# Performance work log

Measured on AMD Instinct MI355X. Metric: run time of the kernel, lower is better.

The kernel has to match this reference:

```python
import jax, jax.numpy as jnp
import numpy as np

B, LA, LS, C, H = 4, 1536, 512, 256, 4
DK = C // H
NEG = -jnp.inf


def _pad(lengths, maxlen):
    # True where padded (idx >= length)
    return jnp.arange(maxlen)[None, :] >= lengths[:, None]


def build_mask(l_v, l_s, ilens, ylens):
    """Additive float mask [B, l_v+l_s, l_v+l_s] with 0 / -inf, matching
    generate_multi_modal_mask_new."""
    b = ilens.shape[0]
    i = jnp.arange(l_s)
    causal = jnp.where(i[:, None] >= i[None, :], 0.0, NEG)            # [l_s, l_s]
    tgt_pad = _pad(ylens, l_s)                                        # [b, l_s]
    mask_s_s = jnp.where(tgt_pad[:, None, :], NEG, causal[None])      # [b, l_s, l_s]
    src_row = jnp.where(_pad(ilens, l_v), NEG, 0.0)                   # [b, l_v]
    mask_v_v = jnp.broadcast_to(src_row[:, None, :], (b, l_v, l_v))
    mask_s_v = jnp.broadcast_to(src_row[:, None, :], (b, l_s, l_v))
    mask_v_s = jnp.full((b, l_v, l_s), NEG, dtype=jnp.float32)
    top = jnp.concatenate([mask_v_v, mask_v_s], axis=2)
    bot = jnp.concatenate([mask_s_v, mask_s_s], axis=2)
    return jnp.concatenate([top, bot], axis=1)


def setup_inputs() -> dict:
    key = jax.random.key(0)
    ks = jax.random.split(key, 12)
    scale = 1.0 / np.sqrt(C)
    return {
        "audio_encoder_out": jax.random.normal(ks[0], (B, LA, C), jnp.float32),
        "text_encoder_out": jax.random.normal(ks[1], (B, LS, C), jnp.float32),
        "speech_length": jax.random.randint(ks[2], (B,), 1, LA),
        "text_length": jax.random.randint(ks[3], (B,), 1, LS),
        "Wq": jax.random.normal(ks[4], (C, C), jnp.float32) * scale,
        "bq": jax.random.normal(ks[5], (C,), jnp.float32) * scale,
        "Wk": jax.random.normal(ks[6], (C, C), jnp.float32) * scale,
        "bk": jax.random.normal(ks[7], (C,), jnp.float32) * scale,
        "Wv": jax.random.normal(ks[8], (C, C), jnp.float32) * scale,
        "bv": jax.random.normal(ks[9], (C,), jnp.float32) * scale,
        "Wo": jax.random.normal(ks[10], (C, C), jnp.float32) * scale,
        "bo": jax.random.normal(ks[11], (C,), jnp.float32) * scale,
    }


def reference(audio_encoder_out, text_encoder_out, speech_length, text_length,
              Wq, bq, Wk, bk, Wv, bv, Wo, bo):
    b, l_a, c = audio_encoder_out.shape
    l_s = text_encoder_out.shape[1]
    x = jnp.concatenate([audio_encoder_out, text_encoder_out], axis=1)  # [B, L, C]
    L = l_a + l_s

    def heads(W, bias):
        return (x @ W.T + bias).reshape(b, L, H, DK).transpose(0, 2, 1, 3)  # [B,H,L,DK]

    q, k, v = heads(Wq, bq), heads(Wk, bk), heads(Wv, bv)
    scores = jnp.einsum("bhqd,bhkd->bhqk", q, k) / np.float32(np.sqrt(DK))

    amask = build_mask(l_a, l_s, speech_length, text_length)  # additive [B,L,L]
    # Faithful to torch: mask.eq(0) positions (additive-0) are filled with -inf,
    # then zeroed in attn (the module's inverted masking behavior).
    eq0 = (amask == 0.0)[:, None, :, :]                       # [B,1,L,L]
    scores = jnp.where(eq0, NEG, scores)
    attn = jax.nn.softmax(scores, axis=-1)
    attn = jnp.where(eq0, 0.0, attn)                          # (dropout = identity, eval)
    out = jnp.einsum("bhqk,bhkd->bhqd", attn, v)
    out = out.transpose(0, 2, 1, 3).reshape(b, L, H * DK)
    return out @ Wo.T + bo
```

## Files before the change

### kernel.cpp

```cpp
#include <hip/hip_runtime.h>
#include <hip/hip_bf16.h>
#include <math.h>

#define LA 1536
#define LS 512
#define LT 2048
#define CC 256
#define NH 4
#define DKH 64
#define NB 4
#define NT (LT / 64)
#define NTA (LA / 64)

typedef _Float16 f16;
typedef __attribute__((ext_vector_type(8))) _Float16 f16x8;
typedef __attribute__((ext_vector_type(4))) _Float16 f16x4;
typedef __attribute__((ext_vector_type(4))) float f32x4;

__device__ inline f16x8 cvt8(const float4 a, const float4 b) {
    f16x8 h;
    h[0] = (_Float16)a.x; h[1] = (_Float16)a.y; h[2] = (_Float16)a.z; h[3] = (_Float16)a.w;
    h[4] = (_Float16)b.x; h[5] = (_Float16)b.y; h[6] = (_Float16)b.z; h[7] = (_Float16)b.w;
    return h;
}

__global__ __launch_bounds__(256) void qkv_mfma(
    const float* __restrict__ audio, const float* __restrict__ text,
    const float* __restrict__ Wq, const float* __restrict__ bq,
    const float* __restrict__ Wk, const float* __restrict__ bk,
    const float* __restrict__ Wv, const float* __restrict__ bv,
    f16* __restrict__ Qh, f16* __restrict__ Kh, f16* __restrict__ Vth)
{
    __shared__ f16 smem[128 * 64 + 64 * 64];
    f16* As = smem;
    f16* Bs = smem + 128 * 64;

    const int tid = threadIdx.x;
    const int w = tid >> 6, l = tid & 63;
    const int g = l >> 4, r = l & 15;

    const int m0 = blockIdx.x * 128;
    const int n0 = blockIdx.y * 64;
    const int mat = n0 >> 8;
    const int ch0 = n0 & 255;

    const float* W    = (mat == 0) ? Wq : (mat == 1) ? Wk : Wv;
    const float* bias = (mat == 0) ? bq : (mat == 1) ? bk : bv;

    const int b  = m0 >> 11;
    const int l0 = m0 & 2047;

    f32x4 acc[2][4] = {};

    for (int k0 = 0; k0 < CC; k0 += 64) {
        #pragma unroll
        for (int m = 0; m < 4; ++m) {
            const int idx = m * 256 + tid;
            const int row = idx >> 3, c = idx & 7;
            const int lrow = l0 + row;
            const float* src = (lrow < LA)
                ? (audio + ((size_t)b * LA + lrow) * CC + k0 + c * 8)
                : (text  + ((size_t)b * LS + (lrow - LA)) * CC + k0 + c * 8);
            const float4 x0 = *(const float4*)src;
            const float4 x1 = *(const float4*)(src + 4);
            *(f16x8*)(As + row * 64 + ((c ^ (row & 7)) << 3)) = cvt8(x0, x1);
        }
        #pragma unroll
        for (int m = 0; m < 2; ++m) {
            const int idx = m * 256 + tid;
            const int row = idx >> 3, c = idx & 7;
            const float* src = W + (size_t)(ch0 + row) * CC + k0 + c * 8;
            const float4 x0 = *(const float4*)src;
            const float4 x1 = *(const float4*)(src + 4);
            *(f16x8*)(Bs + row * 64 + ((c ^ (row & 7)) << 3)) = cvt8(x0, x1);
        }
        __syncthreads();
        #pragma unroll
        for (int kc = 0; kc < 2; ++kc) {
            f16x8 af[2];
            #pragma unroll
            for (int i = 0; i < 2; ++i) {
                const int row = w * 32 + i * 16 + r;
                const int c = kc * 4 + g;
                af[i] = *(const f16x8*)(As + row * 64 + ((c ^ (row & 7)) << 3));
            }
            f16x8 bf[4];
            #pragma unroll
            for (int j = 0; j < 4; ++j) {
                const int row = j * 16 + r;
                const int c = kc * 4 + g;
                bf[j] = *(const f16x8*)(Bs + row * 64 + ((c ^ (row & 7)) << 3));
            }
            #pragma unroll
            for (int i = 0; i < 2; ++i)
                #pragma unroll
                for (int j = 0; j < 4; ++j)
                    acc[i][j] = __builtin_amdgcn_mfma_f32_16x16x32_f16(af[i], bf[j], acc[i][j], 0, 0, 0);
        }
        __syncthreads();
    }

    float bcol[4];
    #pragma unroll
    for (int j = 0; j < 4; ++j) bcol[j] = bias[ch0 + j * 16 + r];

    if (mat <= 1) {
        f16* Out = (mat == 0) ? Qh : Kh;
        #pragma unroll
        for (int i = 0; i < 2; ++i)
            #pragma unroll
            for (int e = 0; e < 4; ++e) {
                const int m = m0 + w * 32 + i * 16 + g * 4 + e;
                #pragma unroll
                for (int j = 0; j < 4; ++j)
                    Out[(size_t)m * CC + ch0 + j * 16 + r] = (_Float16)(acc[i][j][e] + bcol[j]);
            }
    } else {
        f16* Ts = smem;
        #pragma unroll
        for (int i = 0; i < 2; ++i)
            #pragma unroll
            for (int e = 0; e < 4; ++e) {
                const int ml = w * 32 + i * 16 + g * 4 + e;
                #pragma unroll
                for (int j = 0; j < 4; ++j)
                    Ts[(j * 16 + r) * 136 + ml] = (_Float16)(acc[i][j][e] + bcol[j]);
            }
        __syncthreads();
        const int b2 = m0 >> 11, l0m = m0 & 2047;
        #pragma unroll
        for (int u = 0; u < 4; ++u) {
            const int idx = u * 256 + tid;
            const int nl = idx >> 4, mc = idx & 15;
            const f16x8 vv = *(const f16x8*)(Ts + nl * 136 + mc * 8);
            const int nglob = ch0 + nl;
            const int hh = nglob >> 6, dd = nglob & 63;
            *(f16x8*)(Vth + ((size_t)((b2 * NH + hh) * DKH + dd)) * LT + l0m + mc * 8) = vv;
        }
    }
}

__global__ __launch_bounds__(512) void attn_f16(
    const f16* __restrict__ Q, const f16* __restrict__ K,
    const f16* __restrict__ Vt,
    const int* __restrict__ slen, const int* __restrict__ tlen,
    f16* __restrict__ AO)
{
    __shared__ f16 Ks[2][4096];
    __shared__ f16 Vts[2][4096];
    __shared__ f16 Ps[8][16 * 72];
    __shared__ float Oc[4][1024];
    __shared__ float ML[2][64][2];

    const int tid = threadIdx.x;
    const int w = tid >> 6, l = tid & 63;
    const int gid = w >> 2, wg = w & 3;
    const int g = l >> 4, r = l & 15;
    const int tg = tid & 255;

    const int q0 = blockIdx.x * 64;
    const int h  = blockIdx.y;
    const int b  = blockIdx.z;

    const int ilen = slen[b];
    const int kcap = LA + tlen[b];
    const int nskip = ilen >> 6;
    int ntskip = 0;
    if (q0 >= LA) {
        const int skipmax = min(q0 - 63, kcap - 64);
        const int d = skipmax - LA;
        ntskip = (d < 0) ? 0 : ((d >> 6) + 1);
    }
    const int nAudio = NTA - nskip;
    const int nProc  = nAudio + (NT - NTA) - ntskip;
    const int nIter  = (nProc + 1) >> 1;

    const int qrow = q0 + 16 * wg + r;

    f16x8 qf[2];
    #pragma unroll
    for (int ch = 0; ch < 2; ++ch) {
        f16x8 q8 = *(const f16x8*)(Q + ((size_t)(b * LT) + qrow) * CC + h * DKH + ch * 32 + g * 8);
        #pragma unroll
        for (int e = 0; e < 8; ++e) q8[e] = q8[e] * (_Float16)0.125f;
        qf[ch] = q8;
    }

    const int srow0 = tg >> 3, scc = tg & 7;
    const int srow1 = srow0 + 32;
    const int sdst0 = srow0 * 64 + ((scc ^ (srow0 & 7)) << 3);
    const int sdst1 = srow1 * 64 + ((scc ^ (srow1 & 7)) << 3);

    #define TILE_OF(p) ((p) < nAudio ? (nskip + (p)) : (NTA + ntskip + ((p) - nAudio)))

    {
        const int k0 = TILE_OF(gid) * 64;
        *(f16x8*)(Ks[gid] + sdst0)  = *(const f16x8*)(K  + ((size_t)(b * LT) + k0 + srow0) * CC + h * DKH + scc * 8);
        *(f16x8*)(Vts[gid] + sdst0) = *(const f16x8*)(Vt + ((size_t)((b * NH + h) * DKH) + srow0) * LT + k0 + scc * 8);
        *(f16x8*)(Ks[gid] + sdst1)  = *(const f16x8*)(K  + ((size_t)(b * LT) + k0 + srow1) * CC + h * DKH + scc * 8);
        *(f16x8*)(Vts[gid] + sdst1) = *(const f16x8*)(Vt + ((size_t)((b * NH + h) * DKH) + srow1) * LT + k0 + scc * 8);
    }

    float m_run = -1e30f, l_run = 0.0f;
    f32x4 o[4] = {};

    for (int i = 0; i < nIter; ++i) {
        __syncthreads();
        const int pcur = 2 * i + gid;
        const bool curV = pcur < nProc;
        const bool nxtV = (pcur + 2) < nProc;

        f16x8 kr0, vr0, kr1, vr1;
        if (nxtV) {
            const int kn = TILE_OF(pcur + 2) * 64;
            kr0 = *(const f16x8*)(K  + ((size_t)(b * LT) + kn + srow0) * CC + h * DKH + scc * 8);
            vr0 = *(const f16x8*)(Vt + ((size_t)((b * NH + h) * DKH) + srow0) * LT + kn + scc * 8);
            kr1 = *(const f16x8*)(K  + ((size_t)(b * LT) + kn + srow1) * CC + h * DKH + scc * 8);
            vr1 = *(const f16x8*)(Vt + ((size_t)((b * NH + h) * DKH) + srow1) * LT + kn + scc * 8);
        }

        if (curV) {
            const int kt = TILE_OF(pcur);
            const int k0 = kt * 64;

            f32x4 sacc[4] = {};
            #pragma unroll
            for (int s = 0; s < 4; ++s) {
                const int row = 16 * s + r;
                #pragma unroll
                for (int ch = 0; ch < 2; ++ch) {
                    const f16x8 a = *(const f16x8*)(Ks[gid] + row * 64 + ((((ch * 4 + g) ^ (row & 7)) & 7) << 3));
                    sacc[s] = __builtin_amdgcn_mfma_f32_16x16x32_f16(a, qf[ch], sacc[s], 0, 0, 0);
                }
            }

            const int mode = (kt < NTA) ? ((k0 >= ilen) ? 0 : 1)
                                        : ((q0 < LA) ? 0 : 2);
            float sv[16];
            if (mode == 0) {
                #pragma unroll
                for (int s = 0; s < 4; ++s)
                    #pragma unroll
                    for (int e = 0; e < 4; ++e) sv[s * 4 + e] = sacc[s][e];
            } else if (mode == 1) {
                #pragma unroll
                for (int s = 0; s < 4; ++s)
                    #pragma unroll
                    for (int e = 0; e < 4; ++e) {
                        const int kk = k0 + 16 * s + 4 * g + e;
                        sv[s * 4 + e] = (kk >= ilen) ? sacc[s][e] : -INFINITY;
                    }
            } else {
                #pragma unroll
                for (int s = 0; s < 4; ++s)
                    #pragma unroll
                    for (int e = 0; e < 4; ++e) {
                        const int kk = k0 + 16 * s + 4 * g + e;
                        sv[s * 4 + e] = (kk > qrow || kk >= kcap) ? sacc[s][e] : -INFINITY;
                    }
            }

            float mloc = -1e30f;
            #pragma unroll
            for (int u = 0; u < 16; ++u) mloc = fmaxf(mloc, sv[u]);
            mloc = fmaxf(mloc, __shfl_xor(mloc, 16));
            mloc = fmaxf(mloc, __shfl_xor(mloc, 32));
            const float m_new = fmaxf(m_run, mloc);

            float ssum = 0.0f;
            f16x4 ph[4];
            #pragma unroll
            for (int s = 0; s < 4; ++s)
                #pragma unroll
                for (int e = 0; e < 4; ++e) {
                    const float p = __expf(sv[s * 4 + e] - m_new);
                    ph[s][e] = (_Float16)p;
                    ssum += p;
                }
            ssum += __shfl_xor(ssum, 16);
            ssum += __shfl_xor(ssum, 32);
            const float sc = __expf(m_run - m_new);
            l_run = l_run * sc + ssum;
            m_run = m_new;

            #pragma unroll
            for (int s = 0; s < 4; ++s)
                *(f16x4*)(&Ps[w][0] + r * 72 + 16 * s + 4 * g) = ph[s];

            #pragma unroll
            for (int e = 0; e < 4; ++e) {
                const float scr = __shfl(sc, 4 * g + e);
                #pragma unroll
                for (int dsb = 0; dsb < 4; ++dsb) o[dsb][e] *= scr;
            }

            #pragma unroll
            for (int ch = 0; ch < 2; ++ch) {
                const f16x8 a = *(const f16x8*)(&Ps[w][0] + r * 72 + ch * 32 + g * 8);
                #pragma unroll
                for (int dsb = 0; dsb < 4; ++dsb) {
                    const int vrow = 16 * dsb + r;
                    const f16x8 bf = *(const f16x8*)(Vts[gid] + vrow * 64 + ((((ch * 4 + g) ^ (vrow & 7)) & 7) << 3));
                    o[dsb] = __builtin_amdgcn_mfma_f32_16x16x32_f16(a, bf, o[dsb], 0, 0, 0);
                }
            }
        }

        __syncthreads();
        if (nxtV) {
            *(f16x8*)(Ks[gid] + sdst0)  = kr0;
            *(f16x8*)(Vts[gid] + sdst0) = vr0;
            *(f16x8*)(Ks[gid] + sdst1)  = kr1;
            *(f16x8*)(Vts[gid] + sdst1) = vr1;
        }
    }

    if (g == 0) {
        ML[gid][16 * wg + r][0] = m_run;
        ML[gid][16 * wg + r][1] = l_run;
    }
    if (gid == 1) {
        #pragma unroll
        for (int dsb = 0; dsb < 4; ++dsb)
            *(f32x4*)&Oc[wg][dsb * 256 + (g * 16 + r) * 4] = o[dsb];
    }
    __syncthreads();

    if (gid == 0) {
        #pragma unroll
        for (int e = 0; e < 4; ++e) {
            const int qloc = 16 * wg + 4 * g + e;
            const float m0v = ML[0][qloc][0], l0v = ML[0][qloc][1];
            const float m1v = ML[1][qloc][0], l1v = ML[1][qloc][1];
            const float mt = fmaxf(m0v, m1v);
            const float c0 = __expf(m0v - mt);
            const float c1 = __expf(m1v - mt);
            const float inv = 1.0f / (l0v * c0 + l1v * c1);
            const int qq = q0 + qloc;
            #pragma unroll
            for (int dsb = 0; dsb < 4; ++dsb) {
                const float of = (o[dsb][e] * c0 + Oc[wg][dsb * 256 + (g * 16 + r) * 4 + e] * c1) * inv;
                AO[((size_t)(b * LT) + qq) * CC + h * DKH + 16 * dsb + r] = (_Float16)of;
            }
        }
    }
    #undef TILE_OF
}

__global__ __launch_bounds__(256) void out_mfma(
    const f16* __restrict__ X, const float* __restrict__ Wo,
    const float* __restrict__ bo, float* __restrict__ Out)
{
    __shared__ f16 As[128 * 64];
    __shared__ f16 Bs[64 * 64];

    const int tid = threadIdx.x;
    const int w = tid >> 6, l = tid & 63;
    const int g = l >> 4, r = l & 15;

    const int m0 = blockIdx.x * 128;
    const int n0 = blockIdx.y * 64;

    f32x4 acc[2][4] = {};

    for (int k0 = 0; k0 < CC; k0 += 64) {
        #pragma unroll
        for (int m = 0; m < 4; ++m) {
            const int idx = m * 256 + tid;
            const int row = idx >> 3, c = idx & 7;
            *(f16x8*)(As + row * 64 + ((c ^ (row & 7)) << 3)) =
                *(const f16x8*)(X + (size_t)(m0 + row) * CC + k0 + c * 8);
        }
        #pragma unroll
        for (int m = 0; m < 2; ++m) {
            const int idx = m * 256 + tid;
            const int row = idx >> 3, c = idx & 7;
            const float* src = Wo + (size_t)(n0 + row) * CC + k0 + c * 8;
            const float4 x0 = *(const float4*)src;
            const float4 x1 = *(const float4*)(src + 4);
            *(f16x8*)(Bs + row * 64 + ((c ^ (row & 7)) << 3)) = cvt8(x0, x1);
        }
        __syncthreads();
        #pragma unroll
        for (int kc = 0; kc < 2; ++kc) {
            f16x8 af[2];
            #pragma unroll
            for (int i = 0; i < 2; ++i) {
                const int row = w * 32 + i * 16 + r;
                const int c = kc * 4 + g;
                af[i] = *(const f16x8*)(As + row * 64 + ((c ^ (row & 7)) << 3));
            }
            f16x8 bf[4];
            #pragma unroll
            for (int j = 0; j < 4; ++j) {
                const int row = j * 16 + r;
                const int c = kc * 4 + g;
                bf[j] = *(const f16x8*)(Bs + row * 64 + ((c ^ (row & 7)) << 3));
            }
            #pragma unroll
            for (int i = 0; i < 2; ++i)
                #pragma unroll
                for (int j = 0; j < 4; ++j)
                    acc[i][j] = __builtin_amdgcn_mfma_f32_16x16x32_f16(af[i], bf[j], acc[i][j], 0, 0, 0);
        }
        __syncthreads();
    }

    float bcol[4];
    #pragma unroll
    for (int j = 0; j < 4; ++j) bcol[j] = bo[n0 + j * 16 + r];

    #pragma unroll
    for (int i = 0; i < 2; ++i)
        #pragma unroll
        for (int e = 0; e < 4; ++e) {
            const int m = m0 + w * 32 + i * 16 + g * 4 + e;
            #pragma unroll
            for (int j = 0; j < 4; ++j)
                Out[(size_t)m * CC + n0 + j * 16 + r] = acc[i][j][e] + bcol[j];
        }
}

extern "C" void kernel_launch(void* const* d_in, const int* in_sizes, int n_in,
                              void* d_out, int out_size, void* d_ws, size_t ws_size,
                              hipStream_t stream)
{
    const float* audio = (const float*)d_in[0];
    const float* text  = (const float*)d_in[1];
    const int*   slen  = (const int*)d_in[2];
    const int*   tlen  = (const int*)d_in[3];
    const float* Wq = (const float*)d_in[4];
    const float* bq = (const float*)d_in[5];
    const float* Wk = (const float*)d_in[6];
    const float* bk = (const float*)d_in[7];
    const float* Wv = (const float*)d_in[8];
    const float* bv = (const float*)d_in[9];
    const float* Wo = (const float*)d_in[10];
    const float* bo = (const float*)d_in[11];
    float* out = (float*)d_out;

    const size_t SZ = (size_t)NB * LT * CC;
    f16* Qh  = (f16*)d_ws;
    f16* Kh  = Qh + SZ;
    f16* Vth = Kh + SZ;
    f16* AOh = Vth + SZ;

    qkv_mfma<<<dim3(64, 12), 256, 0, stream>>>(audio, text, Wq, bq, Wk, bk, Wv, bv,
                                               Qh, Kh, Vth);
    attn_f16<<<dim3(LT / 64, NH, NB), 512, 0, stream>>>(Qh, Kh, Vth, slen, tlen, AOh);
    out_mfma<<<dim3(64, 4), 256, 0, stream>>>(AOh, Wo, bo, out);
}
```

Before: 49.30 us.

## Give each attention wave two query subtiles, fold scale into Q, use exp2

The attention kernel drops from 512 to 256 threads per block, and each wave now handles 32 query rows instead of 16. This reuses every K and V fragment read from shared memory across two MFMA chains, halving the LDS read traffic per unit of work. The softmax scale times log2(e) is folded into the Q projection epilogue, so the kernel can use exp2f and skip the per-load Q scaling. Rescaling of the running output is skipped when the running max is unchanged across the wave, and the merge buffers now alias the P buffer to cut shared memory. In exchange, register pressure per thread rises and there are fewer waves per block to hide latency.

After: 59.55 us. +20.8%, slower.

```diff
diff --git a/kernel.cpp b/kernel.cpp
--- a/kernel.cpp
+++ b/kernel.cpp
@@ -11,6 +11,9 @@
 #define NB 4
 #define NT (LT / 64)
 #define NTA (LA / 64)
+#define SZ ((size_t)NB * LT * CC)
+
+#define QSCALE 0.1803368801111244f
 
 typedef _Float16 f16;
 typedef __attribute__((ext_vector_type(8))) _Float16 f16x8;
@@ -106,6 +109,7 @@
 
     if (mat <= 1) {
         f16* Out = (mat == 0) ? Qh : Kh;
+        const float osc = (mat == 0) ? QSCALE : 1.0f;
         #pragma unroll
         for (int i = 0; i < 2; ++i)
             #pragma unroll
@@ -113,7 +117,8 @@
                 const int m = m0 + w * 32 + i * 16 + g * 4 + e;
                 #pragma unroll
                 for (int j = 0; j < 4; ++j)
-                    Out[(size_t)m * CC + ch0 + j * 16 + r] = (_Float16)(acc[i][j][e] + bcol[j]);
+                    Out[(size_t)m * CC + ch0 + j * 16 + r] =
+                        (_Float16)((acc[i][j][e] + bcol[j]) * osc);
             }
     } else {
         f16* Ts = smem;
@@ -140,7 +145,7 @@
     }
 }
 
-__global__ __launch_bounds__(512) void attn_f16(
+__global__ __launch_bounds__(256) void attn_f16(
     const f16* __restrict__ Q, const f16* __restrict__ K,
     const f16* __restrict__ Vt,
     const int* __restrict__ slen, const int* __restrict__ tlen,
@@ -148,15 +153,12 @@
 {
     __shared__ f16 Ks[2][4096];
     __shared__ f16 Vts[2][4096];
-    __shared__ f16 Ps[8][16 * 72];
-    __shared__ float Oc[4][1024];
-    __shared__ float ML[2][64][2];
+    __shared__ __align__(16) f16 Ps[4][2304];
 
     const int tid = threadIdx.x;
     const int w = tid >> 6, l = tid & 63;
-    const int gid = w >> 2, wg = w & 3;
+    const int gid = w >> 1, wg = w & 1;
     const int g = l >> 4, r = l & 15;
-    const int tg = tid & 255;
 
     const int q0 = blockIdx.x * 64;
     const int h  = blockIdx.y;
@@ -175,34 +177,37 @@
     const int nProc  = nAudio + (NT - NTA) - ntskip;
     const int nIter  = (nProc + 1) >> 1;
 
-    const int qrow = q0 + 16 * wg + r;
-
-    f16x8 qf[2];
+    const int qbase = q0 + 32 * wg;
+
+    f16x8 qf[2][2];
     #pragma unroll
-    for (int ch = 0; ch < 2; ++ch) {
-        f16x8 q8 = *(const f16x8*)(Q + ((size_t)(b * LT) + qrow) * CC + h * DKH + ch * 32 + g * 8);
-        #pragma unroll
-        for (int e = 0; e < 8; ++e) q8[e] = q8[e] * (_Float16)0.125f;
-        qf[ch] = q8;
-    }
-
-    const int srow0 = tg >> 3, scc = tg & 7;
-    const int srow1 = srow0 + 32;
-    const int sdst0 = srow0 * 64 + ((scc ^ (srow0 & 7)) << 3);
-    const int sdst1 = srow1 * 64 + ((scc ^ (srow1 & 7)) << 3);
+    for (int j = 0; j < 2; ++j)
+        #pragma unroll
+        for (int ch = 0; ch < 2; ++ch)
+            qf[j][ch] = *(const f16x8*)(Q + ((size_t)(b * LT) + qbase + 16 * j + r) * CC
+                                        + h * DKH + ch * 32 + g * 8);
+
+    const int tg = tid & 127;
+    const int rowb = tg >> 3, scc = tg & 7;
+    const int c2 = ((scc ^ (rowb & 7)) << 3);
+    const int sbase = rowb * 64 + c2;
 
     #define TILE_OF(p) ((p) < nAudio ? (nskip + (p)) : (NTA + ntskip + ((p) - nAudio)))
 
     {
         const int k0 = TILE_OF(gid) * 64;
-        *(f16x8*)(Ks[gid] + sdst0)  = *(const f16x8*)(K  + ((size_t)(b * LT) + k0 + srow0) * CC + h * DKH + scc * 8);
-        *(f16x8*)(Vts[gid] + sdst0) = *(const f16x8*)(Vt + ((size_t)((b * NH + h) * DKH) + srow0) * LT + k0 + scc * 8);
-        *(f16x8*)(Ks[gid] + sdst1)  = *(const f16x8*)(K  + ((size_t)(b * LT) + k0 + srow1) * CC + h * DKH + scc * 8);
-        *(f16x8*)(Vts[gid] + sdst1) = *(const f16x8*)(Vt + ((size_t)((b * NH + h) * DKH) + srow1) * LT + k0 + scc * 8);
-    }
-
-    float m_run = -1e30f, l_run = 0.0f;
-    f32x4 o[4] = {};
+        #pragma unroll
+        for (int u = 0; u < 4; ++u) {
+            const int row = u * 16 + rowb;
+            *(f16x8*)(Ks[gid] + u * 1024 + sbase) =
+                *(const f16x8*)(K + ((size_t)(b * LT) + k0 + row) * CC + h * DKH + scc * 8);
+            *(f16x8*)(Vts[gid] + u * 1024 + sbase) =
+                *(const f16x8*)(Vt + ((size_t)((b * NH + h) * DKH) + row) * LT + k0 + scc * 8);
+        }
+    }
+
+    float m_run[2] = {-1e30f, -1e30f}, l_run[2] = {0.0f, 0.0f};
+    f32x4 o[4][2] = {};
 
     for (int i = 0; i < nIter; ++i) {
         __syncthreads();
@@ -210,137 +215,166 @@
         const bool curV = pcur < nProc;
         const bool nxtV = (pcur + 2) < nProc;
 
-        f16x8 kr0, vr0, kr1, vr1;
+        f16x8 kr[4], vr[4];
         if (nxtV) {
             const int kn = TILE_OF(pcur + 2) * 64;
-            kr0 = *(const f16x8*)(K  + ((size_t)(b * LT) + kn + srow0) * CC + h * DKH + scc * 8);
-            vr0 = *(const f16x8*)(Vt + ((size_t)((b * NH + h) * DKH) + srow0) * LT + kn + scc * 8);
-            kr1 = *(const f16x8*)(K  + ((size_t)(b * LT) + kn + srow1) * CC + h * DKH + scc * 8);
-            vr1 = *(const f16x8*)(Vt + ((size_t)((b * NH + h) * DKH) + srow1) * LT + kn + scc * 8);
+            #pragma unroll
+            for (int u = 0; u < 4; ++u) {
+                const int row = u * 16 + rowb;
+                kr[u] = *(const f16x8*)(K + ((size_t)(b * LT) + kn + row) * CC + h * DKH + scc * 8);
+                vr[u] = *(const f16x8*)(Vt + ((size_t)((b * NH + h) * DKH) + row) * LT + kn + scc * 8);
+            }
         }
 
         if (curV) {
             const int kt = TILE_OF(pcur);
             const int k0 = kt * 64;
 
-            f32x4 sacc[4] = {};
+            f32x4 sacc[4][2] = {};
             #pragma unroll
             for (int s = 0; s < 4; ++s) {
-                const int row = 16 * s + r;
+                const int arow = 16 * s + r;
                 #pragma unroll
                 for (int ch = 0; ch < 2; ++ch) {
-                    const f16x8 a = *(const f16x8*)(Ks[gid] + row * 64 + ((((ch * 4 + g) ^ (row & 7)) & 7) << 3));
-                    sacc[s] = __builtin_amdgcn_mfma_f32_16x16x32_f16(a, qf[ch], sacc[s], 0, 0, 0);
+                    const f16x8 a = *(const f16x8*)(Ks[gid] + arow * 64 + ((((ch * 4 + g) ^ (arow & 7)) & 7) << 3));
+                    #pragma unroll
+                    for (int j = 0; j < 2; ++j)
+                        sacc[s][j] = __builtin_amdgcn_mfma_f32_16x16x32_f16(a, qf[j][ch], sacc[s][j], 0, 0, 0);
                 }
             }
 
             const int mode = (kt < NTA) ? ((k0 >= ilen) ? 0 : 1)
                                         : ((q0 < LA) ? 0 : 2);
-            float sv[16];
-            if (mode == 0) {
+
+            #pragma unroll
+            for (int j = 0; j < 2; ++j) {
+                const int qrow = qbase + 16 * j + r;
+                float sv[16];
+                if (mode == 0) {
+                    #pragma unroll
+                    for (int s = 0; s < 4; ++s)
+                        #pragma unroll
+                        for (int e = 0; e < 4; ++e) sv[s * 4 + e] = sacc[s][j][e];
+                } else if (mode == 1) {
+                    #pragma unroll
+                    for (int s = 0; s < 4; ++s)
+                        #pragma unroll
+                        for (int e = 0; e < 4; ++e) {
+                            const int kk = k0 + 16 * s + 4 * g + e;
+                            sv[s * 4 + e] = (kk >= ilen) ? sacc[s][j][e] : -INFINITY;
+                        }
+                } else {
+                    #pragma unroll
+                    for (int s = 0; s < 4; ++s)
+                        #pragma unroll
+                        for (int e = 0; e < 4; ++e) {
+                            const int kk = k0 + 16 * s + 4 * g + e;
+                            sv[s * 4 + e] = (kk > qrow || kk >= kcap) ? sacc[s][j][e] : -INFINITY;
+                        }
+                }
+
+                float mloc = -1e30f;
+                #pragma unroll
+                for (int u = 0; u < 16; ++u) mloc = fmaxf(mloc, sv[u]);
+                mloc = fmaxf(mloc, __shfl_xor(mloc, 16));
+                mloc = fmaxf(mloc, __shfl_xor(mloc, 32));
+                const float m_new = fmaxf(m_run[j], mloc);
+
+                float ssum = 0.0f;
+                f16x4 ph[4];
                 #pragma unroll
                 for (int s = 0; s < 4; ++s)
                     #pragma unroll
-                    for (int e = 0; e < 4; ++e) sv[s * 4 + e] = sacc[s][e];
-            } else if (mode == 1) {
+                    for (int e = 0; e < 4; ++e) {
+                        const float p = exp2f(sv[s * 4 + e] - m_new);
+                        ph[s][e] = (_Float16)p;
+                        ssum += p;
+                    }
+                ssum += __shfl_xor(ssum, 16);
+                ssum += __shfl_xor(ssum, 32);
+
+                if (__all(m_new == m_run[j])) {
+                    l_run[j] += ssum;
+                } else {
+                    const float sc = exp2f(m_run[j] - m_new);
+                    l_run[j] = l_run[j] * sc + ssum;
+                    m_run[j] = m_new;
+                    #pragma unroll
+                    for (int e = 0; e < 4; ++e) {
+                        const float scr = __shfl(sc, 4 * g + e);
+                        #pragma unroll
+                        for (int dsb = 0; dsb < 4; ++dsb) o[dsb][j][e] *= scr;
+                    }
+                }
+
                 #pragma unroll
                 for (int s = 0; s < 4; ++s)
-                    #pragma unroll
-                    for (int e = 0; e < 4; ++e) {
-                        const int kk = k0 + 16 * s + 4 * g + e;
-                        sv[s * 4 + e] = (kk >= ilen) ? sacc[s][e] : -INFINITY;
-                    }
-            } else {
-                #pragma unroll
-                for (int s = 0; s < 4; ++s)
-                    #pragma unroll
-                    for (int e = 0; e < 4; ++e) {
-                        const int kk = k0 + 16 * s + 4 * g + e;
-                        sv[s * 4 + e] = (kk > qrow || kk >= kcap) ? sacc[s][e] : -INFINITY;
-                    }
-            }
-
-            float mloc = -1e30f;
-            #pragma unroll
-            for (int u = 0; u < 16; ++u) mloc = fmaxf(mloc, sv[u]);
-            mloc = fmaxf(mloc, __shfl_xor(mloc, 16));
-            mloc = fmaxf(mloc, __shfl_xor(mloc, 32));
-            const float m_new = fmaxf(m_run, mloc);
-
-            float ssum = 0.0f;
-            f16x4 ph[4];
-            #pragma unroll
-            for (int s = 0; s < 4; ++s)
-                #pragma unroll
-                for (int e = 0; e < 4; ++e) {
-                    const float p = __expf(sv[s * 4 + e] - m_new);
-                    ph[s][e] = (_Float16)p;
-                    ssum += p;
-                }
-            ssum += __shfl_xor(ssum, 16);
-            ssum += __shfl_xor(ssum, 32);
-            const float sc = __expf(m_run - m_new);
-            l_run = l_run * sc + ssum;
-            m_run = m_new;
-
-            #pragma unroll
-            for (int s = 0; s < 4; ++s)
-                *(f16x4*)(&Ps[w][0] + r * 72 + 16 * s + 4 * g) = ph[s];
-
-            #pragma unroll
-            for (int e = 0; e < 4; ++e) {
-                const float scr = __shfl(sc, 4 * g + e);
-                #pragma unroll
-                for (int dsb = 0; dsb < 4; ++dsb) o[dsb][e] *= scr;
+                    *(f16x4*)(&Ps[w][0] + (16 * j + r) * 72 + 16 * s + 4 * g) = ph[s];
             }
 
             #pragma unroll
             for (int ch = 0; ch < 2; ++ch) {
-                const f16x8 a = *(const f16x8*)(&Ps[w][0] + r * 72 + ch * 32 + g * 8);
+                f16x8 a[2];
+                #pragma unroll
+                for (int j = 0; j < 2; ++j)
+                    a[j] = *(const f16x8*)(&Ps[w][0] + (16 * j + r) * 72 + ch * 32 + g * 8);
                 #pragma unroll
                 for (int dsb = 0; dsb < 4; ++dsb) {
                     const int vrow = 16 * dsb + r;
                     const f16x8 bf = *(const f16x8*)(Vts[gid] + vrow * 64 + ((((ch * 4 + g) ^ (vrow & 7)) & 7) << 3));
-                    o[dsb] = __builtin_amdgcn_mfma_f32_16x16x32_f16(a, bf, o[dsb], 0, 0, 0);
+                    #pragma unroll
+                    for (int j = 0; j < 2; ++j)
+                        o[dsb][j] = __builtin_amdgcn_mfma_f32_16x16x32_f16(a[j], bf, o[dsb][j], 0, 0, 0);
                 }
             }
         }
 
         __syncthreads();
         if (nxtV) {
-            *(f16x8*)(Ks[gid] + sdst0)  = kr0;
-            *(f16x8*)(Vts[gid] + sdst0) = vr0;
-            *(f16x8*)(Ks[gid] + sdst1)  = kr1;
-            *(f16x8*)(Vts[gid] + sdst1) = vr1;
-        }
-    }
-
-    if (g == 0) {
-        ML[gid][16 * wg + r][0] = m_run;
-        ML[gid][16 * wg + r][1] = l_run;
-    }
+            #pragma unroll
+            for (int u = 0; u < 4; ++u) {
+                *(f16x8*)(Ks[gid] + u * 1024 + sbase) = kr[u];
+                *(f16x8*)(Vts[gid] + u * 1024 + sbase) = vr[u];
+            }
+        }
+    }
+
+    float* OcF = (float*)&Ps[0][0];
+    float* ML1 = OcF + 4096;
     if (gid == 1) {
         #pragma unroll
-        for (int dsb = 0; dsb < 4; ++dsb)
-            *(f32x4*)&Oc[wg][dsb * 256 + (g * 16 + r) * 4] = o[dsb];
+        for (int j = 0; j < 2; ++j) {
+            #pragma unroll
+            for (int dsb = 0; dsb < 4; ++dsb)
+                *(f32x4*)(OcF + (((wg * 2 + j) * 4 + dsb) << 8) + (l << 2)) = o[dsb][j];
+            if (g == 0) {
+                ML1[(32 * wg + 16 * j + r) * 2 + 0] = m_run[j];
+                ML1[(32 * wg + 16 * j + r) * 2 + 1] = l_run[j];
+            }
+        }
     }
     __syncthreads();
 
     if (gid == 0) {
         #pragma unroll
-        for (int e = 0; e < 4; ++e) {
-            const int qloc = 16 * wg + 4 * g + e;
-            const float m0v = ML[0][qloc][0], l0v = ML[0][qloc][1];
-            const float m1v = ML[1][qloc][0], l1v = ML[1][qloc][1];
-            const float mt = fmaxf(m0v, m1v);
-            const float c0 = __expf(m0v - mt);
-            const float c1 = __expf(m1v - mt);
-            const float inv = 1.0f / (l0v * c0 + l1v * c1);
-            const int qq = q0 + qloc;
-            #pragma unroll
-            for (int dsb = 0; dsb < 4; ++dsb) {
-                const float of = (o[dsb][e] * c0 + Oc[wg][dsb * 256 + (g * 16 + r) * 4 + e] * c1) * inv;
-                AO[((size_t)(b * LT) + qq) * CC + h * DKH + 16 * dsb + r] = (_Float16)of;
+        for (int j = 0; j < 2; ++j) {
+            #pragma unroll
+            for (int e = 0; e < 4; ++e) {
+                const int qloc = 32 * wg + 16 * j + 4 * g + e;
+                const float m0v = __shfl(m_run[j], 4 * g + e);
+                const float l0v = __shfl(l_run[j], 4 * g + e);
+                const float m1v = ML1[qloc * 2 + 0];
+                const float l1v = ML1[qloc * 2 + 1];
+                const float mt = fmaxf(m0v, m1v);
+                const float c0 = exp2f(m0v - mt);
+                const float c1 = exp2f(m1v - mt);
+                const float inv = 1.0f / (l0v * c0 + l1v * c1);
+                #pragma unroll
+                for (int dsb = 0; dsb < 4; ++dsb) {
+                    const float v = (o[dsb][j][e] * c0
+                                   + OcF[(((wg * 2 + j) * 4 + dsb) << 8) + (l << 2) + e] * c1) * inv;
+                    AO[((size_t)(b * LT) + q0 + qloc) * CC + h * DKH + 16 * dsb + r] = (_Float16)v;
+                }
             }
         }
     }
@@ -439,7 +473,6 @@
     const float* bo = (const float*)d_in[11];
     float* out = (float*)d_out;
 
-    const size_t SZ = (size_t)NB * LT * CC;
     f16* Qh  = (f16*)d_ws;
     f16* Kh  = Qh + SZ;
     f16* Vth = Kh + SZ;
@@ -447,6 +480,6 @@
 
     qkv_mfma<<<dim3(64, 12), 256, 0, stream>>>(audio, text, Wq, bq, Wk, bk, Wv, bv,
                                                Qh, Kh, Vth);
-    attn_f16<<<dim3(LT / 64, NH, NB), 512, 0, stream>>>(Qh, Kh, Vth, slen, tlen, AOh);
+    attn_f16<<<dim3(LT / 64, NH, NB), 256, 0, stream>>>(Qh, Kh, Vth, slen, tlen, AOh);
     out_mfma<<<dim3(64, 4), 256, 0, stream>>>(AOh, Wo, bo, out);
 }
```

## Keep P in registers via K row permutation, double-buffer K/V, fold scale into Q

Applied to the files above, without the earlier changes.

Q is pre-scaled by log2(e)/sqrt(dk) in the projection kernel so attention can use exp2 with no per-load scaling. K rows are stored in LDS in a permuted order so the score MFMA output lines up with the PV MFMA A-operand layout. That lets P stay in registers and removes the Ps shared-memory round trip. K/V tiles get a real double buffer with one barrier per iteration instead of two. The output rescale is skipped when no row max changes, and LDS is reused for the final merge. The trade-offs are more shared memory and a more complex index permutation.

New measurement: 51.13 us. +3.7%, slower.

```diff
diff --git a/kernel.cpp b/kernel.cpp
--- a/kernel.cpp
+++ b/kernel.cpp
@@ -11,6 +11,9 @@
 #define NB 4
 #define NT (LT / 64)
 #define NTA (LA / 64)
+#define SZ ((size_t)NB * LT * CC)
+
+#define QSCALE 0.1803368801111244f
 
 typedef _Float16 f16;
 typedef __attribute__((ext_vector_type(8))) _Float16 f16x8;
@@ -23,6 +26,8 @@
     h[4] = (_Float16)b.x; h[5] = (_Float16)b.y; h[6] = (_Float16)b.z; h[7] = (_Float16)b.w;
     return h;
 }
+
+#define PROW(j) (((j) & 32) | ((((j) >> 2) & 1) << 4) | ((((j) >> 3) & 3) << 2) | ((j) & 3))
 
 __global__ __launch_bounds__(256) void qkv_mfma(
     const float* __restrict__ audio, const float* __restrict__ text,
@@ -106,6 +111,7 @@
 
     if (mat <= 1) {
         f16* Out = (mat == 0) ? Qh : Kh;
+        const float osc = (mat == 0) ? QSCALE : 1.0f;
         #pragma unroll
         for (int i = 0; i < 2; ++i)
             #pragma unroll
@@ -113,7 +119,8 @@
                 const int m = m0 + w * 32 + i * 16 + g * 4 + e;
                 #pragma unroll
                 for (int j = 0; j < 4; ++j)
-                    Out[(size_t)m * CC + ch0 + j * 16 + r] = (_Float16)(acc[i][j][e] + bcol[j]);
+                    Out[(size_t)m * CC + ch0 + j * 16 + r] =
+                        (_Float16)((acc[i][j][e] + bcol[j]) * osc);
             }
     } else {
         f16* Ts = smem;
@@ -146,11 +153,8 @@
     const int* __restrict__ slen, const int* __restrict__ tlen,
     f16* __restrict__ AO)
 {
-    __shared__ f16 Ks[2][4096];
-    __shared__ f16 Vts[2][4096];
-    __shared__ f16 Ps[8][16 * 72];
-    __shared__ float Oc[4][1024];
-    __shared__ float ML[2][64][2];
+    __shared__ __align__(16) f16 KsA[2][2 * 4096];
+    __shared__ __align__(16) f16 VtsA[2][2 * 4096];
 
     const int tid = threadIdx.x;
     const int w = tid >> 6, l = tid & 63;
@@ -179,63 +183,70 @@
 
     f16x8 qf[2];
     #pragma unroll
-    for (int ch = 0; ch < 2; ++ch) {
-        f16x8 q8 = *(const f16x8*)(Q + ((size_t)(b * LT) + qrow) * CC + h * DKH + ch * 32 + g * 8);
-        #pragma unroll
-        for (int e = 0; e < 8; ++e) q8[e] = q8[e] * (_Float16)0.125f;
-        qf[ch] = q8;
-    }
+    for (int ch = 0; ch < 2; ++ch)
+        qf[ch] = *(const f16x8*)(Q + ((size_t)(b * LT) + qrow) * CC + h * DKH + ch * 32 + g * 8);
 
     const int srow0 = tg >> 3, scc = tg & 7;
     const int srow1 = srow0 + 32;
-    const int sdst0 = srow0 * 64 + ((scc ^ (srow0 & 7)) << 3);
-    const int sdst1 = srow1 * 64 + ((scc ^ (srow1 & 7)) << 3);
+    const int kp0 = PROW(srow0), kp1 = PROW(srow1);
+    const int kdst0 = kp0 * 64 + ((scc ^ (kp0 & 7)) << 3);
+    const int kdst1 = kp1 * 64 + ((scc ^ (kp1 & 7)) << 3);
+    const int vdst0 = srow0 * 64 + ((scc ^ (srow0 & 7)) << 3);
+    const int vdst1 = srow1 * 64 + ((scc ^ (srow1 & 7)) << 3);
 
     #define TILE_OF(p) ((p) < nAudio ? (nskip + (p)) : (NTA + ntskip + ((p) - nAudio)))
 
     {
         const int k0 = TILE_OF(gid) * 64;
-        *(f16x8*)(Ks[gid] + sdst0)  = *(const f16x8*)(K  + ((size_t)(b * LT) + k0 + srow0) * CC + h * DKH + scc * 8);
-        *(f16x8*)(Vts[gid] + sdst0) = *(const f16x8*)(Vt + ((size_t)((b * NH + h) * DKH) + srow0) * LT + k0 + scc * 8);
-        *(f16x8*)(Ks[gid] + sdst1)  = *(const f16x8*)(K  + ((size_t)(b * LT) + k0 + srow1) * CC + h * DKH + scc * 8);
-        *(f16x8*)(Vts[gid] + sdst1) = *(const f16x8*)(Vt + ((size_t)((b * NH + h) * DKH) + srow1) * LT + k0 + scc * 8);
-    }
+        *(f16x8*)(KsA[gid] + kdst0) =
+            *(const f16x8*)(K + ((size_t)(b * LT) + k0 + srow0) * CC + h * DKH + scc * 8);
+        *(f16x8*)(KsA[gid] + kdst1) =
+            *(const f16x8*)(K + ((size_t)(b * LT) + k0 + srow1) * CC + h * DKH + scc * 8);
+        *(f16x8*)(VtsA[gid] + vdst0) =
+            *(const f16x8*)(Vt + ((size_t)((b * NH + h) * DKH) + srow0) * LT + k0 + scc * 8);
+        *(f16x8*)(VtsA[gid] + vdst1) =
+            *(const f16x8*)(Vt + ((size_t)((b * NH + h) * DKH) + srow1) * LT + k0 + scc * 8);
+    }
+    __syncthreads();
 
     float m_run = -1e30f, l_run = 0.0f;
     f32x4 o[4] = {};
 
+    int cur = 0;
     for (int i = 0; i < nIter; ++i) {
-        __syncthreads();
         const int pcur = 2 * i + gid;
         const bool curV = pcur < nProc;
         const bool nxtV = (pcur + 2) < nProc;
 
-        f16x8 kr0, vr0, kr1, vr1;
+        f16x8 kr0, kr1, vr0, vr1;
         if (nxtV) {
             const int kn = TILE_OF(pcur + 2) * 64;
-            kr0 = *(const f16x8*)(K  + ((size_t)(b * LT) + kn + srow0) * CC + h * DKH + scc * 8);
+            kr0 = *(const f16x8*)(K + ((size_t)(b * LT) + kn + srow0) * CC + h * DKH + scc * 8);
+            kr1 = *(const f16x8*)(K + ((size_t)(b * LT) + kn + srow1) * CC + h * DKH + scc * 8);
             vr0 = *(const f16x8*)(Vt + ((size_t)((b * NH + h) * DKH) + srow0) * LT + kn + scc * 8);
-            kr1 = *(const f16x8*)(K  + ((size_t)(b * LT) + kn + srow1) * CC + h * DKH + scc * 8);
             vr1 = *(const f16x8*)(Vt + ((size_t)((b * NH + h) * DKH) + srow1) * LT + kn + scc * 8);
         }
 
         if (curV) {
             const int kt = TILE_OF(pcur);
             const int k0 = kt * 64;
+            const f16* Kb = KsA[gid] + cur * 4096;
+            const f16* Vb = VtsA[gid] + cur * 4096;
 
             f32x4 sacc[4] = {};
             #pragma unroll
             for (int s = 0; s < 4; ++s) {
-                const int row = 16 * s + r;
+                const int arow = 16 * s + r;
                 #pragma unroll
                 for (int ch = 0; ch < 2; ++ch) {
-                    const f16x8 a = *(const f16x8*)(Ks[gid] + row * 64 + ((((ch * 4 + g) ^ (row & 7)) & 7) << 3));
+                    const f16x8 a = *(const f16x8*)(Kb + arow * 64 + (((ch * 4 + g) ^ (arow & 7)) << 3));
                     sacc[s] = __builtin_amdgcn_mfma_f32_16x16x32_f16(a, qf[ch], sacc[s], 0, 0, 0);
                 }
             }
 
             const int mode = (kt < NTA) ? ((k0 >= ilen) ? 0 : 1)
                                         : ((q0 < LA) ? 0 : 2);
+            const int kb = k0 + 8 * g;
             float sv[16];
             if (mode == 0) {
                 #pragma unroll
@@ -247,7 +258,7 @@
                 for (int s = 0; s < 4; ++s)
                     #pragma unroll
                     for (int e = 0; e < 4; ++e) {
-                        const int kk = k0 + 16 * s + 4 * g + e;
+                        const int kk = kb + 32 * (s >> 1) + 4 * (s & 1) + e;
                         sv[s * 4 + e] = (kk >= ilen) ? sacc[s][e] : -INFINITY;
                     }
             } else {
@@ -255,7 +266,7 @@
                 for (int s = 0; s < 4; ++s)
                     #pragma unroll
                     for (int e = 0; e < 4; ++e) {
-                        const int kk = k0 + 16 * s + 4 * g + e;
+                        const int kk = kb + 32 * (s >> 1) + 4 * (s & 1) + e;
                         sv[s * 4 + e] = (kk > qrow || kk >= kcap) ? sacc[s][e] : -INFINITY;
                     }
             }
@@ -273,56 +284,63 @@
             for (int s = 0; s < 4; ++s)
                 #pragma unroll
                 for (int e = 0; e < 4; ++e) {
-                    const float p = __expf(sv[s * 4 + e] - m_new);
+                    const float p = exp2f(sv[s * 4 + e] - m_new);
                     ph[s][e] = (_Float16)p;
                     ssum += p;
                 }
             ssum += __shfl_xor(ssum, 16);
             ssum += __shfl_xor(ssum, 32);
-            const float sc = __expf(m_run - m_new);
-            l_run = l_run * sc + ssum;
-            m_run = m_new;
-
-            #pragma unroll
-            for (int s = 0; s < 4; ++s)
-                *(f16x4*)(&Ps[w][0] + r * 72 + 16 * s + 4 * g) = ph[s];
-
-            #pragma unroll
-            for (int e = 0; e < 4; ++e) {
-                const float scr = __shfl(sc, 4 * g + e);
-                #pragma unroll
-                for (int dsb = 0; dsb < 4; ++dsb) o[dsb][e] *= scr;
+
+            if (__all(m_new == m_run)) {
+                l_run += ssum;
+            } else {
+                const float sc = exp2f(m_run - m_new);
+                l_run = l_run * sc + ssum;
+                m_run = m_new;
+                #pragma unroll
+                for (int e = 0; e < 4; ++e) {
+                    const float scr = __shfl(sc, 4 * g + e);
+                    #pragma unroll
+                    for (int dsb = 0; dsb < 4; ++dsb) o[dsb][e] *= scr;
+                }
             }
 
             #pragma unroll
             for (int ch = 0; ch < 2; ++ch) {
-                const f16x8 a = *(const f16x8*)(&Ps[w][0] + r * 72 + ch * 32 + g * 8);
+                f16x8 a;
+                #pragma unroll
+                for (int e = 0; e < 4; ++e) { a[e] = ph[2 * ch][e]; a[4 + e] = ph[2 * ch + 1][e]; }
                 #pragma unroll
                 for (int dsb = 0; dsb < 4; ++dsb) {
                     const int vrow = 16 * dsb + r;
-                    const f16x8 bf = *(const f16x8*)(Vts[gid] + vrow * 64 + ((((ch * 4 + g) ^ (vrow & 7)) & 7) << 3));
+                    const f16x8 bf = *(const f16x8*)(Vb + vrow * 64 + (((ch * 4 + g) ^ (vrow & 7)) << 3));
                     o[dsb] = __builtin_amdgcn_mfma_f32_16x16x32_f16(a, bf, o[dsb], 0, 0, 0);
                 }
             }
         }
 
-        __syncthreads();
         if (nxtV) {
-            *(f16x8*)(Ks[gid] + sdst0)  = kr0;
-            *(f16x8*)(Vts[gid] + sdst0) = vr0;
-            *(f16x8*)(Ks[gid] + sdst1)  = kr1;
-            *(f16x8*)(Vts[gid] + sdst1) = vr1;
-        }
-    }
-
-    if (g == 0) {
-        ML[gid][16 * wg + r][0] = m_run;
-        ML[gid][16 * wg + r][1] = l_run;
-    }
+            f16* Kn = KsA[gid] + (cur ^ 1) * 4096;
+            f16* Vn = VtsA[gid] + (cur ^ 1) * 4096;
+            *(f16x8*)(Kn + kdst0) = kr0;
+            *(f16x8*)(Kn + kdst1) = kr1;
+            *(f16x8*)(Vn + vdst0) = vr0;
+            *(f16x8*)(Vn + vdst1) = vr1;
+        }
+        __syncthreads();
+        cur ^= 1;
+    }
+
+    float* OcF = (float*)&KsA[0][0];
+    float* ML1 = (float*)&VtsA[0][0];
     if (gid == 1) {
         #pragma unroll
         for (int dsb = 0; dsb < 4; ++dsb)
-            *(f32x4*)&Oc[wg][dsb * 256 + (g * 16 + r) * 4] = o[dsb];
+            *(f32x4*)(OcF + ((wg * 4 + dsb) << 8) + (l << 2)) = o[dsb];
+        if (g == 0) {
+            ML1[(16 * wg + r) * 2 + 0] = m_run;
+            ML1[(16 * wg + r) * 2 + 1] = l_run;
+        }
     }
     __syncthreads();
 
@@ -330,17 +348,19 @@
         #pragma unroll
         for (int e = 0; e < 4; ++e) {
             const int qloc = 16 * wg + 4 * g + e;
-            const float m0v = ML[0][qloc][0], l0v = ML[0][qloc][1];
-            const float m1v = ML[1][qloc][0], l1v = ML[1][qloc][1];
+            const float m0v = __shfl(m_run, 4 * g + e);
+            const float l0v = __shfl(l_run, 4 * g + e);
+            const float m1v = ML1[qloc * 2 + 0];
+            const float l1v = ML1[qloc * 2 + 1];
             const float mt = fmaxf(m0v, m1v);
-            const float c0 = __expf(m0v - mt);
-            const float c1 = __expf(m1v - mt);
+            const float c0 = exp2f(m0v - mt);
+            const float c1 = exp2f(m1v - mt);
             const float inv = 1.0f / (l0v * c0 + l1v * c1);
-            const int qq = q0 + qloc;
             #pragma unroll
             for (int dsb = 0; dsb < 4; ++dsb) {
-                const float of = (o[dsb][e] * c0 + Oc[wg][dsb * 256 + (g * 16 + r) * 4 + e] * c1) * inv;
-                AO[((size_t)(b * LT) + qq) * CC + h * DKH + 16 * dsb + r] = (_Float16)of;
+                const float v = (o[dsb][e] * c0
+                               + OcF[((wg * 4 + dsb) << 8) + (l << 2) + e] * c1) * inv;
+                AO[((size_t)(b * LT) + q0 + qloc) * CC + h * DKH + 16 * dsb + r] = (_Float16)v;
             }
         }
     }
@@ -439,7 +459,6 @@
     const float* bo = (const float*)d_in[11];
     float* out = (float*)d_out;
 
-    const size_t SZ = (size_t)NB * LT * CC;
     f16* Qh  = (f16*)d_ws;
     f16* Kh  = Qh + SZ;
     f16* Vth = Kh + SZ;
```
